# Kernel tuning notes

Hardware: AMD Instinct MI355X
Metric: run time of the kernel (lower is better)

## Reference

```python
import jax, jax.numpy as jnp
import numpy as np

B, S, F, H = 128, 1024, 512, 128


def setup_inputs() -> dict:
    key = jax.random.key(0)
    ks = jax.random.split(key, 12)
    # ragged valid lengths; force one full-length sequence so padded max == S
    lengths = jax.random.randint(ks[0], (B,), S // 4, S + 1)
    lengths = lengths.at[0].set(S)
    mask = (jnp.arange(S)[None, :] < lengths[:, None]).astype(jnp.float32)
    x = jax.random.normal(ks[1], (B, S, F), jnp.float32) * mask[:, :, None]
    s = 1.0 / np.sqrt(H)

    def u(k, shape):
        return jax.random.uniform(k, shape, jnp.float32, -s, s)

    return {
        "x": x,
        "Wp": u(ks[2], (H, F)), "bp": u(ks[3], (H,)),
        "Wih0": u(ks[4], (3 * H, H)), "Whh0": u(ks[5], (3 * H, H)),
        "bih0": u(ks[6], (3 * H,)), "bhh0": u(ks[7], (3 * H,)),
        "Wih1": u(ks[8], (3 * H, H)), "Whh1": u(ks[9], (3 * H, H)),
        "bih1": u(ks[10], (3 * H,)), "bhh1": u(ks[11], (3 * H,)),
    }


def _gru_layer(xs, Wih, Whh, bih, bhh):
    # xs: [S, B, H_in] -> outputs [S, B, H]; torch nn.GRU gate math (r,z,n order)
    xg = jnp.einsum('sbi,gi->sbg', xs, Wih) + bih  # precompute input gates [S,B,3H]
    Hh = Whh.shape[1]

    def step(h, xg_t):
        hg = h @ Whh.T + bhh
        xr, xz, xn = jnp.split(xg_t, 3, axis=-1)
        hr, hz, hn = jnp.split(hg, 3, axis=-1)
        r = jax.nn.sigmoid(xr + hr)
        z = jax.nn.sigmoid(xz + hz)
        n = jnp.tanh(xn + r * hn)
        h_new = (1.0 - z) * n + z * h
        return h_new, h_new

    h0 = jnp.zeros((xs.shape[1], Hh), xs.dtype)
    _, hs = jax.lax.scan(step, h0, xg)
    return hs


def reference(x, Wp, bp, Wih0, Whh0, bih0, bhh0, Wih1, Whh1, bih1, bhh1):
    # valid lengths: rows whose feature-sum is nonzero
    lengths = (jnp.sum(x, axis=-1) != 0).astype(jnp.int32).sum(axis=1)  # [B]
    proj = x @ Wp.T + bp  # [B,S,H]
    # sort by descending length (module returns outputs in SORTED order, no unsort)
    order = jnp.argsort(-lengths)
    sorted_lengths = lengths[order]
    xs = jnp.transpose(proj[order], (1, 0, 2))  # [S,B,H]
    h1 = _gru_layer(xs, Wih0, Whh0, bih0, bhh0)
    h2 = _gru_layer(h1, Wih1, Whh1, bih1, bhh1)
    out = jnp.transpose(h2, (1, 0, 2))  # [B,S,H]
    # pad_packed_sequence zeros outputs beyond each valid length
    valid = (jnp.arange(S)[None, :] < sorted_lengths[:, None]).astype(out.dtype)
    out = out * valid[:, :, None]
    # mean over padded length (max length == S here), zeros included, as in torch
    return out.mean(axis=1)
```

## Files before the change

### kernel.cpp

```cpp
#include <hip/hip_runtime.h>
#include <hip/hip_bf16.h>

#define BB 128
#define SS 1024
#define FF 512
#define HH 128
#define G3 384

__global__ void zero_len_kernel(int* len) { len[threadIdx.x] = 0; }

__global__ void lengths_kernel(const float* __restrict__ x, int* __restrict__ len) {
    int wave = threadIdx.x >> 6;
    int lane = threadIdx.x & 63;
    long row = (long)blockIdx.x * 4 + wave;
    const float4* p = (const float4*)&x[row * FF + lane * 8];
    float4 v0 = p[0], v1 = p[1];
    float s = v0.x + v0.y + v0.z + v0.w + v1.x + v1.y + v1.z + v1.w;
    #pragma unroll
    for (int off = 32; off > 0; off >>= 1) s += __shfl_down(s, off, 64);
    if (lane == 0 && s != 0.0f) atomicAdd(&len[row >> 10], 1);
}

__global__ void rank_kernel(const int* __restrict__ len, int* __restrict__ rank) {
    int i = threadIdx.x;
    int li = len[i];
    int r = 0;
    for (int jj = 0; jj < BB; jj++) {
        int lj = len[jj];
        if (lj > li || (lj == li && jj < i)) r++;
    }
    rank[i] = r;
}

__global__ __launch_bounds__(256) void gemm_abt(
    const float* __restrict__ A, const float* __restrict__ B,
    const float* __restrict__ bias, float* __restrict__ C,
    int M, int N, int K)
{
    __shared__ float As[16][132];
    __shared__ float Bs[16][132];
    const int tid = threadIdx.x;
    const int tm0 = blockIdx.x * 128;
    const int tn0 = blockIdx.y * 128;
    const int row = tid >> 2;
    const int c4  = (tid & 3) * 4;
    const int ty  = tid >> 4;
    const int tx  = tid & 15;

    float acc[8][8];
    #pragma unroll
    for (int i = 0; i < 8; i++)
        #pragma unroll
        for (int j = 0; j < 8; j++) acc[i][j] = 0.0f;

    for (int k0 = 0; k0 < K; k0 += 16) {
        float4 av0 = *(const float4*)&A[(size_t)(tm0 + row)      * K + k0 + c4];
        float4 av1 = *(const float4*)&A[(size_t)(tm0 + row + 64) * K + k0 + c4];
        float4 bv0 = *(const float4*)&B[(size_t)(tn0 + row)      * K + k0 + c4];
        float4 bv1 = *(const float4*)&B[(size_t)(tn0 + row + 64) * K + k0 + c4];
        __syncthreads();
        As[c4 + 0][row] = av0.x; As[c4 + 1][row] = av0.y;
        As[c4 + 2][row] = av0.z; As[c4 + 3][row] = av0.w;
        As[c4 + 0][row + 64] = av1.x; As[c4 + 1][row + 64] = av1.y;
        As[c4 + 2][row + 64] = av1.z; As[c4 + 3][row + 64] = av1.w;
        Bs[c4 + 0][row] = bv0.x; Bs[c4 + 1][row] = bv0.y;
        Bs[c4 + 2][row] = bv0.z; Bs[c4 + 3][row] = bv0.w;
        Bs[c4 + 0][row + 64] = bv1.x; Bs[c4 + 1][row + 64] = bv1.y;
        Bs[c4 + 2][row + 64] = bv1.z; Bs[c4 + 3][row + 64] = bv1.w;
        __syncthreads();
        #pragma unroll
        for (int kk = 0; kk < 16; kk++) {
            float a[8], b[8];
            *(float4*)&a[0] = *(const float4*)&As[kk][ty * 8];
            *(float4*)&a[4] = *(const float4*)&As[kk][ty * 8 + 4];
            *(float4*)&b[0] = *(const float4*)&Bs[kk][tx * 8];
            *(float4*)&b[4] = *(const float4*)&Bs[kk][tx * 8 + 4];
            #pragma unroll
            for (int i = 0; i < 8; i++)
                #pragma unroll
                for (int j = 0; j < 8; j++)
                    acc[i][j] = fmaf(a[i], b[j], acc[i][j]);
        }
    }

    float bv[8];
    #pragma unroll
    for (int j = 0; j < 8; j++) bv[j] = bias[tn0 + tx * 8 + j];
    #pragma unroll
    for (int i = 0; i < 8; i++) {
        size_t crow = (size_t)(tm0 + ty * 8 + i) * N + tn0 + tx * 8;
        float4 o0, o1;
        o0.x = acc[i][0] + bv[0]; o0.y = acc[i][1] + bv[1];
        o0.z = acc[i][2] + bv[2]; o0.w = acc[i][3] + bv[3];
        o1.x = acc[i][4] + bv[4]; o1.y = acc[i][5] + bv[5];
        o1.z = acc[i][6] + bv[6]; o1.w = acc[i][7] + bv[7];
        *(float4*)&C[crow]     = o0;
        *(float4*)&C[crow + 4] = o1;
    }
}

__device__ __forceinline__ float fast_sigmoid(float x) {
    return __builtin_amdgcn_rcpf(1.0f + __expf(-x));
}
__device__ __forceinline__ float fast_tanh(float x) {
    return 1.0f - 2.0f * __builtin_amdgcn_rcpf(1.0f + __expf(2.0f * x));
}

template<int FINAL>
__global__ __launch_bounds__(512, 2) __attribute__((amdgpu_waves_per_eu(2, 2)))
void gru_rec(
    const float* __restrict__ xg,
    const float* __restrict__ Whh,
    const float* __restrict__ bhh,
    float* __restrict__ h_out,
    const int* __restrict__ len,
    const int* __restrict__ rank)
{
    const int b   = blockIdx.x;
    const int tid = threadIdx.x;
    const int j   = tid >> 2;
    const int kq  = tid & 3;

    __shared__ __align__(16) float h_lds[2][HH];

    float4 wv[3][8];
    #pragma unroll
    for (int g = 0; g < 3; g++) {
        const float4* wr = (const float4*)&Whh[(size_t)(g * HH + j) * HH + kq * 32];
        #pragma unroll
        for (int q = 0; q < 8; q++) wv[g][q] = wr[(q + 2 * kq) & 7];
    }
    #pragma unroll
    for (int g = 0; g < 3; g++)
        #pragma unroll
        for (int q = 0; q < 8; q++)
            asm volatile("" : "+v"(wv[g][q].x), "+v"(wv[g][q].y),
                              "+v"(wv[g][q].z), "+v"(wv[g][q].w));

    float b_r = 0.f, b_z = 0.f, b_n = 0.f;
    if (kq == 0) { b_r = bhh[j]; b_z = bhh[HH + j]; b_n = bhh[2 * HH + j]; }
    const float* xgb = xg + (size_t)b * SS * G3;

    if (tid < 2 * HH) ((float*)h_lds)[tid] = 0.0f;
    float hprev = 0.0f, osum = 0.0f;
    const int L = FINAL ? len[b] : 0;

    float xr = 0.f, xz = 0.f, xn = 0.f;
    if (kq == 0) { xr = xgb[j]; xz = xgb[HH + j]; xn = xgb[2 * HH + j]; }
    __syncthreads();

    for (int t = 0; t < SS; t++) {
        if (!FINAL && t > 0 && tid >= 64 && tid < 96) {
            int c = tid - 64;
            float4 hv = ((const float4*)h_lds[t & 1])[c];
            *(float4*)&h_out[((size_t)b * SS + (t - 1)) * HH + c * 4] = hv;
        }
        float nxr = 0.f, nxz = 0.f, nxn = 0.f;
        if (kq == 0 && t + 1 < SS) {
            const float* p = xgb + (size_t)(t + 1) * G3;
            nxr = p[j]; nxz = p[HH + j]; nxn = p[2 * HH + j];
        }
        const float4* h4 = (const float4*)h_lds[t & 1];
        float4 ar = {0,0,0,0}, az = {0,0,0,0}, an = {0,0,0,0};
        #pragma unroll
        for (int q = 0; q < 8; q++) {
            float4 hv = h4[kq * 8 + ((q + 2 * kq) & 7)];
            float4 w0 = wv[0][q], w1 = wv[1][q], w2 = wv[2][q];
            ar.x = fmaf(w0.x, hv.x, ar.x); ar.y = fmaf(w0.y, hv.y, ar.y);
            ar.z = fmaf(w0.z, hv.z, ar.z); ar.w = fmaf(w0.w, hv.w, ar.w);
            az.x = fmaf(w1.x, hv.x, az.x); az.y = fmaf(w1.y, hv.y, az.y);
            az.z = fmaf(w1.z, hv.z, az.z); az.w = fmaf(w1.w, hv.w, az.w);
            an.x = fmaf(w2.x, hv.x, an.x); an.y = fmaf(w2.y, hv.y, an.y);
            an.z = fmaf(w2.z, hv.z, an.z); an.w = fmaf(w2.w, hv.w, an.w);
        }
        float a0 = (ar.x + ar.y) + (ar.z + ar.w);
        float a1 = (az.x + az.y) + (az.z + az.w);
        float a2 = (an.x + an.y) + (an.z + an.w);
        a0 += __shfl_xor(a0, 1, 64); a1 += __shfl_xor(a1, 1, 64); a2 += __shfl_xor(a2, 1, 64);
        a0 += __shfl_xor(a0, 2, 64); a1 += __shfl_xor(a1, 2, 64); a2 += __shfl_xor(a2, 2, 64);
        if (kq == 0) {
            float r = fast_sigmoid(xr + a0 + b_r);
            float z = fast_sigmoid(xz + a1 + b_z);
            float n = fast_tanh(xn + r * (a2 + b_n));
            float h = (1.0f - z) * n + z * hprev;
            hprev = h;
            h_lds[(t + 1) & 1][j] = h;
            if (FINAL) { if (t < L) osum += h; }
        }
        xr = nxr; xz = nxz; xn = nxn;
        __syncthreads();
    }
    if (!FINAL && tid >= 64 && tid < 96) {
        int c = tid - 64;
        float4 hv = ((const float4*)h_lds[SS & 1])[c];
        *(float4*)&h_out[((size_t)b * SS + (SS - 1)) * HH + c * 4] = hv;
    }
    if (FINAL && kq == 0) {
        h_out[(size_t)rank[b] * HH + j] = osum * (1.0f / (float)SS);
    }
}

extern "C" void kernel_launch(void* const* d_in, const int* in_sizes, int n_in,
                              void* d_out, int out_size, void* d_ws, size_t ws_size,
                              hipStream_t stream) {
    const float* x    = (const float*)d_in[0];
    const float* Wp   = (const float*)d_in[1];
    const float* bp   = (const float*)d_in[2];
    const float* Wih0 = (const float*)d_in[3];
    const float* Whh0 = (const float*)d_in[4];
    const float* bih0 = (const float*)d_in[5];
    const float* bhh0 = (const float*)d_in[6];
    const float* Wih1 = (const float*)d_in[7];
    const float* Whh1 = (const float*)d_in[8];
    const float* bih1 = (const float*)d_in[9];
    const float* bhh1 = (const float*)d_in[10];
    float* out = (float*)d_out;

    int* len  = (int*)d_ws;
    int* rank = len + 128;
    float* proj = (float*)((char*)d_ws + 4096);
    float* xgb  = proj + (size_t)BB * SS * HH;

    zero_len_kernel<<<1, 128, 0, stream>>>(len);
    lengths_kernel<<<(BB * SS) / 4, 256, 0, stream>>>(x, len);
    rank_kernel<<<1, 128, 0, stream>>>(len, rank);

    gemm_abt<<<dim3(BB * SS / 128, HH / 128), 256, 0, stream>>>(x, Wp, bp, proj,
                                                               BB * SS, HH, FF);
    gemm_abt<<<dim3(BB * SS / 128, G3 / 128), 256, 0, stream>>>(proj, Wih0, bih0, xgb,
                                                                BB * SS, G3, HH);
    gru_rec<0><<<BB, 512, 0, stream>>>(xgb, Whh0, bhh0, proj, len, rank);

    gemm_abt<<<dim3(BB * SS / 128, G3 / 128), 256, 0, stream>>>(proj, Wih1, bih1, xgb,
                                                                BB * SS, G3, HH);
    gru_rec<1><<<BB, 512, 0, stream>>>(xgb, Whh1, bhh1, out, len, rank);
}
```

Baseline: 2.391 ms.

## Replace FP32 SIMT projection GEMMs with split-bf16 MFMA GEMM

The projection and input-gate GEMMs move from a scalar FMA tiled kernel to an MFMA 16x16x32 bf16 kernel. Each fp32 operand is split into high and low bf16 parts, and three MFMA products keep close to fp32 accuracy. Weights are converted into LDS on every k-step and A fragments are loaded directly from global memory. This trades extra conversion work and uncoalesced scalar output stores for much higher matrix throughput. The recurrence kernel's launch attributes are also rewritten in an equivalent form.

```diff
diff --git a/kernel.cpp b/kernel.cpp
--- a/kernel.cpp
+++ b/kernel.cpp
@@ -6,6 +6,9 @@
 #define FF 512
 #define HH 128
 #define G3 384
+
+typedef __attribute__((ext_vector_type(8))) short bf16x8;
+typedef __attribute__((ext_vector_type(4))) float f32x4;
 
 __global__ void zero_len_kernel(int* len) { len[threadIdx.x] = 0; }
 
@@ -32,70 +35,89 @@
     rank[i] = r;
 }
 
-__global__ __launch_bounds__(256) void gemm_abt(
-    const float* __restrict__ A, const float* __restrict__ B,
+__device__ __forceinline__ short bf_hi(float w, float& hf) {
+    unsigned u = __builtin_bit_cast(unsigned, w);
+    unsigned r = (u + 0x7FFFu + ((u >> 16) & 1u)) & 0xFFFF0000u;
+    hf = __builtin_bit_cast(float, r);
+    return (short)(r >> 16);
+}
+__device__ __forceinline__ short bf_rn(float w) {
+    unsigned u = __builtin_bit_cast(unsigned, w);
+    unsigned r = u + 0x7FFFu + ((u >> 16) & 1u);
+    return (short)(r >> 16);
+}
+
+__global__ __launch_bounds__(256) void gemm_mfma(
+    const float* __restrict__ A, const float* __restrict__ W,
     const float* __restrict__ bias, float* __restrict__ C,
     int M, int N, int K)
 {
-    __shared__ float As[16][132];
-    __shared__ float Bs[16][132];
-    const int tid = threadIdx.x;
-    const int tm0 = blockIdx.x * 128;
-    const int tn0 = blockIdx.y * 128;
-    const int row = tid >> 2;
-    const int c4  = (tid & 3) * 4;
-    const int ty  = tid >> 4;
-    const int tx  = tid & 15;
-
-    float acc[8][8];
-    #pragma unroll
-    for (int i = 0; i < 8; i++)
-        #pragma unroll
-        for (int j = 0; j < 8; j++) acc[i][j] = 0.0f;
-
-    for (int k0 = 0; k0 < K; k0 += 16) {
-        float4 av0 = *(const float4*)&A[(size_t)(tm0 + row)      * K + k0 + c4];
-        float4 av1 = *(const float4*)&A[(size_t)(tm0 + row + 64) * K + k0 + c4];
-        float4 bv0 = *(const float4*)&B[(size_t)(tn0 + row)      * K + k0 + c4];
-        float4 bv1 = *(const float4*)&B[(size_t)(tn0 + row + 64) * K + k0 + c4];
+    const int tid  = threadIdx.x;
+    const int wvid = tid >> 6;
+    const int lane = tid & 63;
+    const int m0   = blockIdx.x * 64 + wvid * 16;
+    const int n0   = blockIdx.y * 128;
+    const int KS   = K >> 5;
+
+    __shared__ __align__(16) short sh[2][8][64][8];
+
+    f32x4 acc[8];
+    #pragma unroll
+    for (int i = 0; i < 8; i++) acc[i] = (f32x4){0.f, 0.f, 0.f, 0.f};
+
+    const int arow = m0 + (lane & 15);
+    const int koff = (lane >> 4) << 3;
+
+    for (int ks = 0; ks < KS; ks++) {
         __syncthreads();
-        As[c4 + 0][row] = av0.x; As[c4 + 1][row] = av0.y;
-        As[c4 + 2][row] = av0.z; As[c4 + 3][row] = av0.w;
-        As[c4 + 0][row + 64] = av1.x; As[c4 + 1][row + 64] = av1.y;
-        As[c4 + 2][row + 64] = av1.z; As[c4 + 3][row + 64] = av1.w;
-        Bs[c4 + 0][row] = bv0.x; Bs[c4 + 1][row] = bv0.y;
-        Bs[c4 + 2][row] = bv0.z; Bs[c4 + 3][row] = bv0.w;
-        Bs[c4 + 0][row + 64] = bv1.x; Bs[c4 + 1][row + 64] = bv1.y;
-        Bs[c4 + 2][row + 64] = bv1.z; Bs[c4 + 3][row + 64] = bv1.w;
+        #pragma unroll
+        for (int i = 0; i < 2; i++) {
+            int p  = tid + i * 256;
+            int nt = p >> 6, ln = p & 63;
+            const float* src = &W[(size_t)(n0 + nt * 16 + (ln & 15)) * K
+                                  + ks * 32 + ((ln >> 4) << 3)];
+            float w8[8];
+            *(float4*)&w8[0] = *(const float4*)&src[0];
+            *(float4*)&w8[4] = *(const float4*)&src[4];
+            short hi8[8], lo8[8];
+            #pragma unroll
+            for (int e = 0; e < 8; e++) {
+                float hf; hi8[e] = bf_hi(w8[e], hf);
+                lo8[e] = bf_rn(w8[e] - hf);
+            }
+            *(bf16x8*)&sh[0][nt][ln][0] = *(bf16x8*)hi8;
+            *(bf16x8*)&sh[1][nt][ln][0] = *(bf16x8*)lo8;
+        }
+        const float* ap = &A[(size_t)arow * K + ks * 32 + koff];
+        float av[8];
+        *(float4*)&av[0] = *(const float4*)&ap[0];
+        *(float4*)&av[4] = *(const float4*)&ap[4];
+        short ah[8], al[8];
+        #pragma unroll
+        for (int e = 0; e < 8; e++) {
+            float hf; ah[e] = bf_hi(av[e], hf);
+            al[e] = bf_rn(av[e] - hf);
+        }
+        bf16x8 ahi = *(bf16x8*)ah, alo = *(bf16x8*)al;
         __syncthreads();
         #pragma unroll
-        for (int kk = 0; kk < 16; kk++) {
-            float a[8], b[8];
-            *(float4*)&a[0] = *(const float4*)&As[kk][ty * 8];
-            *(float4*)&a[4] = *(const float4*)&As[kk][ty * 8 + 4];
-            *(float4*)&b[0] = *(const float4*)&Bs[kk][tx * 8];
-            *(float4*)&b[4] = *(const float4*)&Bs[kk][tx * 8 + 4];
-            #pragma unroll
-            for (int i = 0; i < 8; i++)
-                #pragma unroll
-                for (int j = 0; j < 8; j++)
-                    acc[i][j] = fmaf(a[i], b[j], acc[i][j]);
-        }
-    }
-
-    float bv[8];
-    #pragma unroll
-    for (int j = 0; j < 8; j++) bv[j] = bias[tn0 + tx * 8 + j];
-    #pragma unroll
-    for (int i = 0; i < 8; i++) {
-        size_t crow = (size_t)(tm0 + ty * 8 + i) * N + tn0 + tx * 8;
-        float4 o0, o1;
-        o0.x = acc[i][0] + bv[0]; o0.y = acc[i][1] + bv[1];
-        o0.z = acc[i][2] + bv[2]; o0.w = acc[i][3] + bv[3];
-        o1.x = acc[i][4] + bv[4]; o1.y = acc[i][5] + bv[5];
-        o1.z = acc[i][6] + bv[6]; o1.w = acc[i][7] + bv[7];
-        *(float4*)&C[crow]     = o0;
-        *(float4*)&C[crow + 4] = o1;
+        for (int nt = 0; nt < 8; nt++) {
+            bf16x8 bhi = *(bf16x8*)&sh[0][nt][lane][0];
+            bf16x8 blo = *(bf16x8*)&sh[1][nt][lane][0];
+            acc[nt] = __builtin_amdgcn_mfma_f32_16x16x32_bf16(ahi, bhi, acc[nt], 0, 0, 0);
+            acc[nt] = __builtin_amdgcn_mfma_f32_16x16x32_bf16(ahi, blo, acc[nt], 0, 0, 0);
+            acc[nt] = __builtin_amdgcn_mfma_f32_16x16x32_bf16(alo, bhi, acc[nt], 0, 0, 0);
+        }
+    }
+    const int crow = m0 + ((lane >> 4) << 2);
+    const int ccol = n0 + (lane & 15);
+    #pragma unroll
+    for (int nt = 0; nt < 8; nt++) {
+        int col = ccol + nt * 16;
+        float bv = bias[col];
+        #pragma unroll
+        for (int r = 0; r < 4; r++)
+            C[(size_t)(crow + r) * N + col] = acc[nt][r] + bv;
     }
 }
 
@@ -107,7 +129,7 @@
 }
 
 template<int FINAL>
-__global__ __launch_bounds__(512, 2) __attribute__((amdgpu_waves_per_eu(2, 2)))
+__global__ __attribute__((amdgpu_flat_work_group_size(512, 512), amdgpu_waves_per_eu(2, 2)))
 void gru_rec(
     const float* __restrict__ xg,
     const float* __restrict__ Whh,
@@ -225,13 +247,13 @@
     lengths_kernel<<<(BB * SS) / 4, 256, 0, stream>>>(x, len);
     rank_kernel<<<1, 128, 0, stream>>>(len, rank);
 
-    gemm_abt<<<dim3(BB * SS / 128, HH / 128), 256, 0, stream>>>(x, Wp, bp, proj,
-                                                               BB * SS, HH, FF);
-    gemm_abt<<<dim3(BB * SS / 128, G3 / 128), 256, 0, stream>>>(proj, Wih0, bih0, xgb,
-                                                                BB * SS, G3, HH);
+    gemm_mfma<<<dim3(BB * SS / 64, 1), 256, 0, stream>>>(x, Wp, bp, proj,
+                                                         BB * SS, HH, FF);
+    gemm_mfma<<<dim3(BB * SS / 64, 3), 256, 0, stream>>>(proj, Wih0, bih0, xgb,
+                                                         BB * SS, G3, HH);
     gru_rec<0><<<BB, 512, 0, stream>>>(xgb, Whh0, bhh0, proj, len, rank);
 
-    gemm_abt<<<dim3(BB * SS / 128, G3 / 128), 256, 0, stream>>>(proj, Wih1, bih1, xgb,
-                                                                BB * SS, G3, HH);
+    gemm_mfma<<<dim3(BB * SS / 64, 3), 256, 0, stream>>>(proj, Wih1, bih1, xgb,
+                                                         BB * SS, G3, HH);
     gru_rec<1><<<BB, 512, 0, stream>>>(xgb, Whh1, bhh1, out, len, rank);
 }
```

New measurement: 1.979 ms. 1.21x faster.
